# Kernel tuning notes

Measured on AMD Instinct MI355X. Metric: run time of the kernel, lower is better.

The kernel has to match this reference:

```python
import jax, jax.numpy as jnp
import numpy as np

B, S, D = 4, 2048, 2048
NQ, NKV = 16, 4
HD = D // NQ          # head_size = 128
GROUP = NQ // NKV     # 4


def _rope_table(seq_len, head_size, theta=10000.0):
    # [seq, head_size/2, 2] = (cos, sin), matching torch polar freqs_cis
    inv = 1.0 / (theta ** (np.arange(0, head_size, 2, dtype=np.float32) / head_size))
    ang = np.arange(seq_len, dtype=np.float32)[:, None] * inv[None, :]
    return jnp.asarray(np.stack([np.cos(ang), np.sin(ang)], axis=-1))


def setup_inputs() -> dict:
    key = jax.random.key(0)
    ks = jax.random.split(key, 6)
    sd = 0.02
    return {
        "x": jax.random.normal(ks[0], (B, S, D), jnp.float32),
        "freq_cis": _rope_table(S, HD),
        "Wq": jax.random.normal(ks[1], (D, NQ * HD), jnp.float32) * sd,
        "bq": jnp.zeros((NQ * HD,), jnp.float32),
        "Wk": jax.random.normal(ks[2], (D, NKV * HD), jnp.float32) * sd,
        "bk": jnp.zeros((NKV * HD,), jnp.float32),
        "Wv": jax.random.normal(ks[3], (D, NKV * HD), jnp.float32) * sd,
        "bv": jnp.zeros((NKV * HD,), jnp.float32),
        "Wo": jax.random.normal(ks[4], (NQ * HD, D), jnp.float32) * sd,
        "start_pos": 0,
    }


def _apply_rope(x, fc):
    # x: [b, s, h, d]; fc: [s, d/2, 2] -> complex multiply on (even, odd) pairs
    xr = x.reshape(*x.shape[:-1], -1, 2)
    cos = fc[None, :, None, :, 0]
    sin = fc[None, :, None, :, 1]
    x0, x1 = xr[..., 0], xr[..., 1]
    out = jnp.stack([x0 * cos - x1 * sin, x0 * sin + x1 * cos], axis=-1)
    return out.reshape(x.shape)


def reference(x, freq_cis, Wq, bq, Wk, bk, Wv, bv, Wo, start_pos):
    b, s, _ = x.shape
    q = (x @ Wq + bq).reshape(b, s, NQ, HD)
    k = (x @ Wk + bk).reshape(b, s, NKV, HD)
    v = (x @ Wv + bv).reshape(b, s, NKV, HD)

    fc = freq_cis[start_pos:start_pos + s]
    q = _apply_rope(q, fc)
    k = _apply_rope(k, fc)

    # [b, nkv, group, s, d] query view; k/v stay [b, nkv, s, d] (GQA broadcast)
    q = q.transpose(0, 2, 1, 3).reshape(b, NKV, GROUP, s, HD)
    k = k.transpose(0, 2, 1, 3)
    v = v.transpose(0, 2, 1, 3)

    scale = 1.0 / jnp.sqrt(jnp.asarray(HD, x.dtype))
    scores = jnp.einsum("bhgqd,bhkd->bhgqk", q, k) * scale
    causal = jnp.tril(jnp.ones((s, s), bool))
    scores = jnp.where(causal[None, None, None], scores, jnp.asarray(-jnp.inf, scores.dtype))
    probs = jax.nn.softmax(scores, axis=-1)
    o = jnp.einsum("bhgqk,bhkd->bhgqd", probs, v)

    o = o.reshape(b, NQ, s, HD).transpose(0, 2, 1, 3).reshape(b, s, NQ * HD)
    return o @ Wo
```

## Files before the change

### kernel.cpp

```cpp
#include <hip/hip_runtime.h>
#include <stdint.h>

typedef __attribute__((ext_vector_type(8))) short bf16x8;
typedef __attribute__((ext_vector_type(4))) float f32x4;
typedef __attribute__((ext_vector_type(16))) float f32x16;

#define S_LEN 2048
#define D_MODEL 2048
#define NQH 16
#define NKVH 4
#define HDIM 128
#define BATCH 4

__device__ __forceinline__ float bf2f(unsigned short s) {
  union { unsigned u; float f; } v; v.u = ((unsigned)s) << 16; return v.f;
}
__device__ __forceinline__ unsigned short f2bf(float f) {
  union { float f; unsigned u; } v; v.f = f;
  unsigned r = v.u + 0x7FFFu + ((v.u >> 16) & 1u);
  return (unsigned short)(r >> 16);
}
__device__ __forceinline__ f32x4 fzero() {
  f32x4 v; v[0]=0.f; v[1]=0.f; v[2]=0.f; v[3]=0.f; return v;
}
__device__ __forceinline__ void async16(const void* g, void* l) {
  __builtin_amdgcn_global_load_lds(
      (const __attribute__((address_space(1))) unsigned int*)g,
      (__attribute__((address_space(3))) unsigned int*)l, 16, 0, 0);
}
__device__ __forceinline__ unsigned cvtpk(float lo, float hi) {
  unsigned r;
  asm("v_cvt_pk_bf16_f32 %0, %1, %2" : "=v"(r) : "v"(lo), "v"(hi));
  return r;
}

__global__ void k_convert_x(const float* __restrict__ x, unsigned short* __restrict__ xb, int n4) {
  int stride = gridDim.x * blockDim.x;
  for (int i = blockIdx.x * blockDim.x + threadIdx.x; i < n4; i += stride) {
    float4 v = ((const float4*)x)[i];
    ushort4 o;
    o.x = f2bf(v.x); o.y = f2bf(v.y); o.z = f2bf(v.z); o.w = f2bf(v.w);
    ((ushort4*)xb)[i] = o;
  }
}

__global__ void k_transpose_all(const float* __restrict__ Wq, const float* __restrict__ Wk,
                                const float* __restrict__ Wv, const float* __restrict__ Wo,
                                unsigned short* __restrict__ Wt, unsigned short* __restrict__ Wot) {
  __shared__ float tile[32][33];
  int bid = blockIdx.x;
  const float* W; unsigned short* D; int N, nx;
  if (bid < 4096)      { W = Wq; D = Wt;                          N = 2048; nx = 64; }
  else if (bid < 5120) { W = Wk; D = Wt + (size_t)2048 * 2048;    N = 512;  nx = 16; bid -= 4096; }
  else if (bid < 6144) { W = Wv; D = Wt + (size_t)2560 * 2048;    N = 512;  nx = 16; bid -= 5120; }
  else                 { W = Wo; D = Wot;                         N = 2048; nx = 64; bid -= 6144; }
  int tx = threadIdx.x & 31, ty = threadIdx.x >> 5;
  int n0 = (bid % nx) * 32, k0 = (bid / nx) * 32;
  #pragma unroll
  for (int i = 0; i < 4; ++i)
    tile[ty + i*8][tx] = W[(size_t)(k0 + ty + i*8) * N + n0 + tx];
  __syncthreads();
  #pragma unroll
  for (int i = 0; i < 4; ++i)
    D[(size_t)(n0 + ty + i*8) * 2048 + k0 + tx] = f2bf(tile[tx][ty + i*8]);
}

__global__ void k_rope2(unsigned short* __restrict__ Qb, unsigned short* __restrict__ Kb,
                        const float* __restrict__ fc, const int* __restrict__ start_pos,
                        int nq, int ntot) {
  int sp = start_pos[0];
  int stride = gridDim.x * blockDim.x;
  for (int i = blockIdx.x * blockDim.x + threadIdx.x; i < ntot; i += stride) {
    unsigned* T = (i < nq) ? (unsigned*)Qb : (unsigned*)Kb;
    int idx = (i < nq) ? i : i - nq;
    int d2 = idx & 63;
    int s = (idx >> 6) & (S_LEN - 1);
    unsigned v = T[idx];
    float x0 = bf2f((unsigned short)(v & 0xFFFFu));
    float x1 = bf2f((unsigned short)(v >> 16));
    float c  = fc[((size_t)(sp + s) * 64 + d2) * 2];
    float sn = fc[((size_t)(sp + s) * 64 + d2) * 2 + 1];
    float y0 = x0 * c - x1 * sn;
    float y1 = x0 * sn + x1 * c;
    T[idx] = (unsigned)f2bf(y0) | ((unsigned)f2bf(y1) << 16);
  }
}

#define BARRIER() __builtin_amdgcn_s_barrier()
#define LGKM0()  do { asm volatile("s_waitcnt lgkmcnt(0)" ::: "memory"); \
                      __builtin_amdgcn_sched_barrier(0); } while (0)
#define VMCNT6() asm volatile("s_waitcnt vmcnt(6)" ::: "memory")
#define VMCNT4() asm volatile("s_waitcnt vmcnt(4)" ::: "memory")
#define VMCNT0() asm volatile("s_waitcnt vmcnt(0)" ::: "memory")

__device__ __forceinline__ bf16x8 ldsrd(const unsigned short* L, int row, int kk, int g) {
  int Xs = (kk * 64 + g * 16) ^ ((row & 7) << 4);
  return *(const bf16x8*)&L[row * 64 + (Xs >> 1)];
}
__device__ __forceinline__ void stage8(const unsigned short* __restrict__ G, int gbase,
                                       int k0, unsigned short* lds, int rowbase, int lane) {
  int row = rowbase + (lane >> 3);
  int col8 = (lane & 7) ^ ((lane >> 3) & 7);
  async16(G + (size_t)(gbase + row) * 2048 + k0 + col8 * 8, lds + rowbase * 64 + lane * 8);
}

__global__ __launch_bounds__(512, 2) void k_gemm_qkv(
    const unsigned short* __restrict__ A, const unsigned short* __restrict__ Bt,
    const float* __restrict__ bq, const float* __restrict__ bk, const float* __restrict__ bv,
    unsigned short* __restrict__ Qo, unsigned short* __restrict__ Ko, unsigned short* __restrict__ Vto)
{
  __shared__ __align__(16) unsigned short Ab[3][256 * 64];
  __shared__ __align__(16) unsigned short Bb[3][128 * 64];
  const int NT = 32, NXT = 24;
  const int tid = threadIdx.x, lane = tid & 63, w = tid >> 6;
  const int lr = lane & 15, g = lane >> 4;
  const int wm = w >> 1, wn = w & 1;

  int nwg = NXT * 32;
  int cpx = nwg >> 3;
  int bid = blockIdx.x;
  int swz = (bid & 7) * cpx + (bid >> 3);
  const int by = swz / NXT, bx = swz % NXT;
  const int mbase = by * 256, nbase = bx * 128;

  #define ST_A(tt) { unsigned short* L = Ab[(tt) % 3]; int k0 = (tt) * 64; \
    _Pragma("unroll") for (int it = 0; it < 4; ++it) { int c = tid + it * 512; \
      int row = c >> 3, col8 = (c & 7) ^ (row & 7); \
      async16(A + (size_t)(mbase + row) * 2048 + k0 + col8 * 8, L + c * 8); } }
  #define ST_B(tt) { unsigned short* L = Bb[(tt) % 3]; int k0 = (tt) * 64; \
    _Pragma("unroll") for (int it = 0; it < 2; ++it) { int c = tid + it * 512; \
      int row = c >> 3, col8 = (c & 7) ^ (row & 7); \
      async16(Bt + (size_t)(nbase + row) * 2048 + k0 + col8 * 8, L + c * 8); } }

  f32x4 acc[4][4];
  #pragma unroll
  for (int m = 0; m < 4; ++m)
    #pragma unroll
    for (int n = 0; n < 4; ++n) acc[m][n] = fzero();

  ST_A(0); ST_B(0); ST_A(1); ST_B(1);
  VMCNT6();
  BARRIER();

  for (int t = 0; t < NT; ++t) {
    const unsigned short* Al = Ab[t % 3];
    const unsigned short* Bl = Bb[t % 3];
    bf16x8 a[2][4], b[2][2];

    #pragma unroll
    for (int kk = 0; kk < 2; ++kk) {
      #pragma unroll
      for (int m = 0; m < 4; ++m) a[kk][m] = ldsrd(Al, wm * 64 + m * 16 + lr, kk, g);
      #pragma unroll
      for (int n = 0; n < 2; ++n) b[kk][n] = ldsrd(Bl, wn * 64 + n * 16 + lr, kk, g);
    }
    if (t + 2 < NT) ST_A(t + 2);
    BARRIER(); LGKM0();
    __builtin_amdgcn_s_setprio(1);
    #pragma unroll
    for (int kk = 0; kk < 2; ++kk)
      #pragma unroll
      for (int m = 0; m < 4; ++m)
        #pragma unroll
        for (int n = 0; n < 2; ++n)
          acc[m][n] = __builtin_amdgcn_mfma_f32_16x16x32_bf16(a[kk][m], b[kk][n], acc[m][n], 0, 0, 0);
    __builtin_amdgcn_s_setprio(0);
    BARRIER();

    #pragma unroll
    for (int kk = 0; kk < 2; ++kk)
      #pragma unroll
      for (int n = 0; n < 2; ++n) b[kk][n] = ldsrd(Bl, wn * 64 + (2 + n) * 16 + lr, kk, g);
    if (t + 2 < NT) { ST_B(t + 2); VMCNT6(); } else { VMCNT0(); }
    BARRIER(); LGKM0();
    __builtin_amdgcn_s_setprio(1);
    #pragma unroll
    for (int kk = 0; kk < 2; ++kk)
      #pragma unroll
      for (int m = 0; m < 4; ++m)
        #pragma unroll
        for (int n = 0; n < 2; ++n)
          acc[m][2 + n] = __builtin_amdgcn_mfma_f32_16x16x32_bf16(a[kk][m], b[kk][n], acc[m][2 + n], 0, 0, 0);
    __builtin_amdgcn_s_setprio(0);
    BARRIER();
  }

  const float SCL2E = 0.08838834764831845f * 1.4426950408889634f;
  #pragma unroll
  for (int n = 0; n < 4; ++n) {
    const int ng = nbase + wn * 64 + n * 16 + lr;
    const int seg = (ng < 2048) ? 0 : (ng < 2560 ? 1 : 2);
    const int nn = ng - (seg == 0 ? 0 : (seg == 1 ? 2048 : 2560));
    const int hh = nn >> 7, dd = nn & 127;
    const float bias = (seg == 0 ? bq[nn] : (seg == 1 ? bk[nn] : bv[nn]));
    #pragma unroll
    for (int m = 0; m < 4; ++m)
      #pragma unroll
      for (int i = 0; i < 4; ++i) {
        int mg = mbase + wm * 64 + m * 16 + g * 4 + i;
        int bb = mg >> 11, s = mg & 2047;
        float val = acc[m][n][i] + bias;
        if (seg == 0) {
          val *= SCL2E;
          Qo[((size_t)(bb * NQH + hh) * S_LEN + s) * HDIM + dd] = f2bf(val);
        } else if (seg == 1) {
          Ko[((size_t)(bb * NKVH + hh) * S_LEN + s) * HDIM + dd] = f2bf(val);
        } else {
          Vto[((size_t)(bb * NKVH + hh) * HDIM + dd) * S_LEN + s] = f2bf(val);
        }
      }
  }
  #undef ST_A
  #undef ST_B
}

__global__ __launch_bounds__(512, 2) void k_gemm_out256(
    const unsigned short* __restrict__ A, const unsigned short* __restrict__ Bt,
    float* __restrict__ Cf)
{
  __shared__ __align__(16) unsigned short Abuf[2][256 * 64];
  __shared__ __align__(16) unsigned short Bbuf[2][256 * 64];
  const int NT = 32, NXT = 8;
  const int tid = threadIdx.x, lane = tid & 63, w = tid >> 6;
  const int lr = lane & 15, g = lane >> 4;
  const int wm = w >> 2, wn = w & 3;

  int nwg = NXT * 32;
  int cpx = nwg >> 3;
  int bid = blockIdx.x;
  int swz = (bid & 7) * cpx + (bid >> 3);
  const int by = swz / NXT, bx = swz % NXT;
  const int mbase = by * 256, nbase = bx * 256;

  #define ST_AQ02(tt) if ((tt) < NT) { unsigned short* L = Abuf[(tt) & 1]; int k0 = (tt) * 64; \
    _Pragma("unroll") for (int it = 0; it < 2; ++it) { int sub = it * 8 + w; \
      stage8(A, mbase, k0, L, (sub >> 3) * 128 + (sub & 7) * 8, lane); } }
  #define ST_AQ13(tt) if ((tt) < NT) { unsigned short* L = Abuf[(tt) & 1]; int k0 = (tt) * 64; \
    _Pragma("unroll") for (int it = 0; it < 2; ++it) { int sub = it * 8 + w; \
      stage8(A, mbase, k0, L, 64 + (sub >> 3) * 128 + (sub & 7) * 8, lane); } }
  #define ST_BS0(tt) if ((tt) < NT) { unsigned short* L = Bbuf[(tt) & 1]; int k0 = (tt) * 64; \
    _Pragma("unroll") for (int it = 0; it < 2; ++it) { int sub = it * 8 + w; \
      stage8(Bt, nbase, k0, L, (sub >> 2) * 64 + (sub & 3) * 8, lane); } }
  #define ST_BS1(tt) if ((tt) < NT) { unsigned short* L = Bbuf[(tt) & 1]; int k0 = (tt) * 64; \
    _Pragma("unroll") for (int it = 0; it < 2; ++it) { int sub = it * 8 + w; \
      stage8(Bt, nbase, k0, L, 32 + (sub >> 2) * 64 + (sub & 3) * 8, lane); } }

  f32x4 acc[8][4];
  #pragma unroll
  for (int m = 0; m < 8; ++m)
    #pragma unroll
    for (int n = 0; n < 4; ++n) acc[m][n] = fzero();

  ST_AQ02(0); ST_AQ13(0); ST_BS0(0); ST_BS1(0);
  ST_AQ02(1); ST_BS1(1);
  VMCNT4();
  BARRIER();

  bf16x8 a[2][4], b[2][2];

  for (int t = 0; t < NT; ++t) {
    const unsigned short* Al = Abuf[t & 1];
    const unsigned short* Bl = Bbuf[t & 1];

    #pragma unroll
    for (int kk = 0; kk < 2; ++kk) {
      #pragma unroll
      for (int m = 0; m < 4; ++m) a[kk][m] = ldsrd(Al, wm * 128 + m * 16 + lr, kk, g);
      #pragma unroll
      for (int n = 0; n < 2; ++n) b[kk][n] = ldsrd(Bl, wn * 64 + n * 16 + lr, kk, g);
    }
    ST_AQ13(t + 1);
    BARRIER(); LGKM0();
    __builtin_amdgcn_s_setprio(1);
    #pragma unroll
    for (int kk = 0; kk < 2; ++kk)
      #pragma unroll
      for (int m = 0; m < 4; ++m)
        #pragma unroll
        for (int n = 0; n < 2; ++n)
          acc[m][n] = __builtin_amdgcn_mfma_f32_16x16x32_bf16(a[kk][m], b[kk][n], acc[m][n], 0, 0, 0);
    __builtin_amdgcn_s_setprio(0);
    BARRIER();

    #pragma unroll
    for (int kk = 0; kk < 2; ++kk)
      #pragma unroll
      for (int n = 0; n < 2; ++n) b[kk][n] = ldsrd(Bl, wn * 64 + (2 + n) * 16 + lr, kk, g);
    ST_BS0(t + 1);
    BARRIER(); LGKM0();
    __builtin_amdgcn_s_setprio(1);
    #pragma unroll
    for (int kk = 0; kk < 2; ++kk)
      #pragma unroll
      for (int m = 0; m < 4; ++m)
        #pragma unroll
        for (int n = 0; n < 2; ++n)
          acc[m][2 + n] = __builtin_amdgcn_mfma_f32_16x16x32_bf16(a[kk][m], b[kk][n], acc[m][2 + n], 0, 0, 0);
    __builtin_amdgcn_s_setprio(0);
    BARRIER();

    #pragma unroll
    for (int kk = 0; kk < 2; ++kk)
      #pragma unroll
      for (int m = 0; m < 4; ++m) a[kk][m] = ldsrd(Al, wm * 128 + 64 + m * 16 + lr, kk, g);
    ST_AQ02(t + 2);
    BARRIER(); LGKM0();
    __builtin_amdgcn_s_setprio(1);
    #pragma unroll
    for (int kk = 0; kk < 2; ++kk)
      #pragma unroll
      for (int m = 0; m < 4; ++m)
        #pragma unroll
        for (int n = 0; n < 2; ++n)
          acc[4 + m][2 + n] = __builtin_amdgcn_mfma_f32_16x16x32_bf16(a[kk][m], b[kk][n], acc[4 + m][2 + n], 0, 0, 0);
    __builtin_amdgcn_s_setprio(0);
    BARRIER();

    #pragma unroll
    for (int kk = 0; kk < 2; ++kk)
      #pragma unroll
      for (int n = 0; n < 2; ++n) b[kk][n] = ldsrd(Bl, wn * 64 + n * 16 + lr, kk, g);
    ST_BS1(t + 2);
    VMCNT4();
    BARRIER(); LGKM0();
    __builtin_amdgcn_s_setprio(1);
    #pragma unroll
    for (int kk = 0; kk < 2; ++kk)
      #pragma unroll
      for (int m = 0; m < 4; ++m)
        #pragma unroll
        for (int n = 0; n < 2; ++n)
          acc[4 + m][n] = __builtin_amdgcn_mfma_f32_16x16x32_bf16(a[kk][m], b[kk][n], acc[4 + m][n], 0, 0, 0);
    __builtin_amdgcn_s_setprio(0);
    BARRIER();
  }

  #pragma unroll
  for (int m = 0; m < 8; ++m)
    #pragma unroll
    for (int n = 0; n < 4; ++n)
      #pragma unroll
      for (int i = 0; i < 4; ++i) {
        int mg = mbase + wm * 128 + m * 16 + g * 4 + i;
        int ng = nbase + wn * 64 + n * 16 + lr;
        Cf[(size_t)mg * 2048 + ng] = acc[m][n][i];
      }
  #undef ST_AQ02
  #undef ST_AQ13
  #undef ST_BS0
  #undef ST_BS1
}

__global__ __launch_bounds__(512, 2) void k_flash2(
    const unsigned short* __restrict__ Q, const unsigned short* __restrict__ K,
    const unsigned short* __restrict__ Vt, unsigned short* __restrict__ O)
{
  __shared__ __align__(16) unsigned short SH[49152];

  const int tid = threadIdx.x;
  const int lane = tid & 63;
  const int w = tid >> 6;
  const int ql = lane & 31;
  const int hi = lane >> 5;

  const int bh = blockIdx.x >> 2;
  const int tp = blockIdx.x & 3;
  const int b = bh >> 4, h = bh & 15;
  const int kh = h >> 2;

  const unsigned short* Qbase = Q + (size_t)(b * NQH + h) * S_LEN * HDIM;
  const unsigned short* Kbase = K + (size_t)(b * NKVH + kh) * S_LEN * HDIM;
  const unsigned short* Vtb   = Vt + (size_t)(b * NKVH + kh) * HDIM * S_LEN;

  #define STAGEKV(jj) { unsigned short* Kd = SH + ((jj) % 3) * 16384; \
    unsigned short* Vd = Kd + 8192; \
    _Pragma("unroll") for (int it = 0; it < 2; ++it) { \
      int c = tid + it * 512; int row = c >> 4, col = c & 15; \
      int lcol = (col & 8) | ((col ^ (row & 7)) & 7); \
      async16(Kbase + (size_t)((jj) * 64 + row) * HDIM + lcol * 8, Kd + c * 8); } \
    _Pragma("unroll") for (int it = 0; it < 2; ++it) { \
      int c = tid + it * 512; int row = c >> 3, col = c & 7; \
      int lcol = col ^ (row & 7); \
      async16(Vtb + (size_t)row * S_LEN + (jj) * 64 + lcol * 8, Vd + c * 8); } }

  #pragma unroll 1
  for (int half = 0; half < 2; ++half) {
    const int t = half ? (7 - tp) : tp;
    const int nkv = 4 * t + 4;
    const int qg = t * 256 + w * 32 + ql;

    __syncthreads();

    bf16x8 qf[8];
    {
      const unsigned short* qp = Qbase + (size_t)qg * HDIM;
      #pragma unroll
      for (int dd = 0; dd < 8; ++dd)
        qf[dd] = *(const bf16x8*)(qp + dd * 16 + hi * 8);
    }

    float m_r = -1e30f, l_r = 0.f;
    f32x16 oA[4];
    #pragma unroll
    for (int db = 0; db < 4; ++db)
      #pragma unroll
      for (int r = 0; r < 16; ++r) oA[db][r] = 0.f;

    STAGEKV(0);
    STAGEKV(1);
    VMCNT4();
    BARRIER();

    for (int j = 0; j < nkv; ++j) {
      const unsigned short* Kl = SH + (j % 3) * 16384;
      const unsigned short* Vl = Kl + 8192;

      if (j + 2 < nkv) STAGEKV(j + 2);

      if (j * 64 <= t * 256 + w * 32 + 31) {
        f32x16 p0, p1;
        #pragma unroll
        for (int r = 0; r < 16; ++r) { p0[r] = 0.f; p1[r] = 0.f; }
        __builtin_amdgcn_s_setprio(1);
        #pragma unroll
        for (int dd = 0; dd < 8; ++dd) {
          const int off = (((dd * 32 + hi * 16) ^ ((ql & 7) << 4)) >> 1);
          bf16x8 a0 = *(const bf16x8*)&Kl[ql * 128 + off];
          bf16x8 a1 = *(const bf16x8*)&Kl[(32 + ql) * 128 + off];
          p0 = __builtin_amdgcn_mfma_f32_32x32x16_bf16(a0, qf[dd], p0, 0, 0, 0);
          p1 = __builtin_amdgcn_mfma_f32_32x32x16_bf16(a1, qf[dd], p1, 0, 0, 0);
        }
        __builtin_amdgcn_s_setprio(0);

        #pragma unroll
        for (int r = 0; r < 16; ++r) {
          const int kl = (r & 3) + 8 * (r >> 2);
          int kg = j * 64 + kl + 4 * hi;
          if (kg > qg) p0[r] = -1e30f;
          if (kg + 32 > qg) p1[r] = -1e30f;
        }

        float pm = -1e30f;
        #pragma unroll
        for (int r = 0; r < 16; ++r) pm = fmaxf(pm, fmaxf(p0[r], p1[r]));
        pm = fmaxf(pm, __shfl_xor(pm, 32));
        if (!__all(pm - m_r <= 8.0f)) {
          const float mn = fmaxf(m_r, pm);
          const float corr = exp2f(m_r - mn);
          m_r = mn;
          l_r *= corr;
          #pragma unroll
          for (int db = 0; db < 4; ++db)
            #pragma unroll
            for (int r = 0; r < 16; ++r) oA[db][r] *= corr;
        }
        float rs = 0.f;
        #pragma unroll
        for (int r = 0; r < 16; ++r) {
          p0[r] = exp2f(p0[r] - m_r);
          p1[r] = exp2f(p1[r] - m_r);
          rs += p0[r] + p1[r];
        }
        rs += __shfl_xor(rs, 32);
        l_r += rs;

        bf16x8 pb[4];
        {
          unsigned Wv[8], W2v[8];
          #pragma unroll
          for (int d = 0; d < 4; ++d) {
            Wv[d]      = cvtpk(p0[4*d],     p0[4*d + 1]);
            W2v[d]     = cvtpk(p0[4*d + 2], p0[4*d + 3]);
            Wv[4 + d]  = cvtpk(p1[4*d],     p1[4*d + 1]);
            W2v[4 + d] = cvtpk(p1[4*d + 2], p1[4*d + 3]);
          }
          #pragma unroll
          for (int kt = 0; kt < 2; ++kt) {
            #pragma unroll
            for (int s = 0; s < 2; ++s) {
              unsigned ownW   = hi ? Wv[kt*4 + 2*s + 1]  : Wv[kt*4 + 2*s];
              unsigned sendW  = hi ? Wv[kt*4 + 2*s]      : Wv[kt*4 + 2*s + 1];
              unsigned recvW  = (unsigned)__shfl_xor((int)sendW, 32);
              unsigned ownW2  = hi ? W2v[kt*4 + 2*s + 1] : W2v[kt*4 + 2*s];
              unsigned sendW2 = hi ? W2v[kt*4 + 2*s]     : W2v[kt*4 + 2*s + 1];
              unsigned recvW2 = (unsigned)__shfl_xor((int)sendW2, 32);
              union { unsigned u[4]; bf16x8 v; } pk;
              pk.u[0] = hi ? recvW  : ownW;
              pk.u[1] = hi ? recvW2 : ownW2;
              pk.u[2] = hi ? ownW   : recvW;
              pk.u[3] = hi ? ownW2  : recvW2;
              pb[kt*2 + s] = pk.v;
            }
          }
        }

        __builtin_amdgcn_s_setprio(1);
        #pragma unroll
        for (int ks = 0; ks < 4; ++ks) {
          #pragma unroll
          for (int db = 0; db < 4; ++db) {
            const int off = (((ks * 32 + hi * 16) ^ ((ql & 7) << 4)) >> 1);
            bf16x8 av = *(const bf16x8*)&Vl[(db * 32 + ql) * 64 + off];
            oA[db] = __builtin_amdgcn_mfma_f32_32x32x16_bf16(av, pb[ks], oA[db], 0, 0, 0);
          }
        }
        __builtin_amdgcn_s_setprio(0);
      }

      if (j + 2 < nkv) { VMCNT4(); }
      else if (j + 1 < nkv) { VMCNT0(); }
      BARRIER();
    }

    {
      const float invl = 1.f / l_r;
      const int qloc = w * 32 + ql;
      #pragma unroll
      for (int db = 0; db < 4; ++db)
        #pragma unroll
        for (int g4 = 0; g4 < 4; ++g4) {
          unsigned lo  = cvtpk(oA[db][g4*4 + 0] * invl, oA[db][g4*4 + 1] * invl);
          unsigned hi2 = cvtpk(oA[db][g4*4 + 2] * invl, oA[db][g4*4 + 3] * invl);
          int byteoff = qloc * 256 + ((db * 64 + g4 * 16 + hi * 8) ^ ((qloc & 7) << 4));
          *(uint2*)((char*)SH + byteoff) = make_uint2(lo, hi2);
        }
    }
    __syncthreads();
    {
      const int q2 = tid >> 1, hf = tid & 1;
      unsigned short* orow = O + ((size_t)(b * S_LEN + t * 256 + q2)) * D_MODEL + h * HDIM + hf * 64;
      #pragma unroll
      for (int u = 0; u < 8; ++u) {
        int byteoff = q2 * 256 + ((hf * 128 + u * 16) ^ ((q2 & 7) << 4));
        bf16x8 v = *(const bf16x8*)((const char*)SH + byteoff);
        *(bf16x8*)(orow + u * 8) = v;
      }
    }
  }
  #undef STAGEKV
}

extern "C" void kernel_launch(void* const* d_in, const int* in_sizes, int n_in,
                              void* d_out, int out_size, void* d_ws, size_t ws_size,
                              hipStream_t stream) {
  (void)in_sizes; (void)n_in; (void)out_size; (void)ws_size;
  const float* x  = (const float*)d_in[0];
  const float* fc = (const float*)d_in[1];
  const float* Wq = (const float*)d_in[2];
  const float* bq = (const float*)d_in[3];
  const float* Wk = (const float*)d_in[4];
  const float* bk = (const float*)d_in[5];
  const float* Wv = (const float*)d_in[6];
  const float* bv = (const float*)d_in[7];
  const float* Wo = (const float*)d_in[8];
  const int* start_pos = (const int*)d_in[9];
  float* out = (float*)d_out;

  unsigned short* ws = (unsigned short*)d_ws;
  size_t off = 0;
  unsigned short* xb  = ws + off; off += (size_t)8192 * 2048;
  unsigned short* Wt  = ws + off; off += (size_t)3072 * 2048;
  unsigned short* Wot = ws + off; off += (size_t)2048 * 2048;
  unsigned short* Qb  = ws + off; off += (size_t)BATCH * NQH  * S_LEN * HDIM;
  unsigned short* Kb  = ws + off; off += (size_t)BATCH * NKVH * S_LEN * HDIM;
  unsigned short* Vtb = ws + off; off += (size_t)BATCH * NKVH * S_LEN * HDIM;
  unsigned short* Ob  = ws + off; off += (size_t)8192 * 2048;

  k_convert_x<<<2048, 256, 0, stream>>>(x, xb, 8192 * 2048 / 4);
  k_transpose_all<<<10240, 256, 0, stream>>>(Wq, Wk, Wv, Wo, Wt, Wot);

  k_gemm_qkv<<<dim3(768), 512, 0, stream>>>(xb, Wt, bq, bk, bv, Qb, Kb, Vtb);

  k_rope2<<<2048, 256, 0, stream>>>(Qb, Kb, fc, start_pos,
                                    BATCH * NQH * S_LEN * 64,
                                    (BATCH * NQH + BATCH * NKVH) * S_LEN * 64);

  k_flash2<<<dim3(256), 512, 0, stream>>>(Qb, Kb, Vtb, Ob);

  k_gemm_out256<<<dim3(256), 512, 0, stream>>>(Ob, Wot, out);
}
```

Baseline: 373.6 us.

## Fuse Q RoPE into flash attention and shrink attention blocks to 128 queries

RoPE for Q now runs inside the flash kernel while Q fragments are loaded, so the separate pass no longer reads and writes Q through global memory. RoPE for K stays in a smaller standalone kernel. The flash kernel moves from 512 threads with 256-query tiles and triple-buffered KV to 256 threads with 128-query tiles, double buffering and a full barrier each iteration, and launches twice as many blocks. This trades Q global traffic and launch cost for a shallower prefetch pipeline, more barrier stalls, and extra RoPE arithmetic and fc loads in the attention kernel.

```diff
diff --git a/kernel.cpp b/kernel.cpp
--- a/kernel.cpp
+++ b/kernel.cpp
@@ -65,24 +65,21 @@
     D[(size_t)(n0 + ty + i*8) * 2048 + k0 + tx] = f2bf(tile[tx][ty + i*8]);
 }
 
-__global__ void k_rope2(unsigned short* __restrict__ Qb, unsigned short* __restrict__ Kb,
-                        const float* __restrict__ fc, const int* __restrict__ start_pos,
-                        int nq, int ntot) {
+__global__ void k_ropeK(unsigned short* __restrict__ Kb, const float* __restrict__ fc,
+                        const int* __restrict__ start_pos, int total) {
   int sp = start_pos[0];
   int stride = gridDim.x * blockDim.x;
-  for (int i = blockIdx.x * blockDim.x + threadIdx.x; i < ntot; i += stride) {
-    unsigned* T = (i < nq) ? (unsigned*)Qb : (unsigned*)Kb;
-    int idx = (i < nq) ? i : i - nq;
-    int d2 = idx & 63;
-    int s = (idx >> 6) & (S_LEN - 1);
-    unsigned v = T[idx];
+  for (int i = blockIdx.x * blockDim.x + threadIdx.x; i < total; i += stride) {
+    int d2 = i & 63;
+    int s = (i >> 6) & (S_LEN - 1);
+    unsigned v = ((unsigned*)Kb)[i];
     float x0 = bf2f((unsigned short)(v & 0xFFFFu));
     float x1 = bf2f((unsigned short)(v >> 16));
     float c  = fc[((size_t)(sp + s) * 64 + d2) * 2];
     float sn = fc[((size_t)(sp + s) * 64 + d2) * 2 + 1];
     float y0 = x0 * c - x1 * sn;
     float y1 = x0 * sn + x1 * c;
-    T[idx] = (unsigned)f2bf(y0) | ((unsigned)f2bf(y1) << 16);
+    ((unsigned*)Kb)[i] = (unsigned)f2bf(y0) | ((unsigned)f2bf(y1) << 16);
   }
 }
 
@@ -90,7 +87,6 @@
 #define LGKM0()  do { asm volatile("s_waitcnt lgkmcnt(0)" ::: "memory"); \
                       __builtin_amdgcn_sched_barrier(0); } while (0)
 #define VMCNT6() asm volatile("s_waitcnt vmcnt(6)" ::: "memory")
-#define VMCNT4() asm volatile("s_waitcnt vmcnt(4)" ::: "memory")
 #define VMCNT0() asm volatile("s_waitcnt vmcnt(0)" ::: "memory")
 
 __device__ __forceinline__ bf16x8 ldsrd(const unsigned short* L, int row, int kk, int g) {
@@ -253,7 +249,7 @@
 
   ST_AQ02(0); ST_AQ13(0); ST_BS0(0); ST_BS1(0);
   ST_AQ02(1); ST_BS1(1);
-  VMCNT4();
+  asm volatile("s_waitcnt vmcnt(4)" ::: "memory");
   BARRIER();
 
   bf16x8 a[2][4], b[2][2];
@@ -321,7 +317,7 @@
       #pragma unroll
       for (int n = 0; n < 2; ++n) b[kk][n] = ldsrd(Bl, wn * 64 + n * 16 + lr, kk, g);
     ST_BS1(t + 2);
-    VMCNT4();
+    asm volatile("s_waitcnt vmcnt(4)" ::: "memory");
     BARRIER(); LGKM0();
     __builtin_amdgcn_s_setprio(1);
     #pragma unroll
@@ -351,11 +347,12 @@
   #undef ST_BS1
 }
 
-__global__ __launch_bounds__(512, 2) void k_flash2(
+__global__ __launch_bounds__(256, 2) void k_flash2(
     const unsigned short* __restrict__ Q, const unsigned short* __restrict__ K,
-    const unsigned short* __restrict__ Vt, unsigned short* __restrict__ O)
+    const unsigned short* __restrict__ Vt, unsigned short* __restrict__ O,
+    const float* __restrict__ fc, const int* __restrict__ start_pos)
 {
-  __shared__ __align__(16) unsigned short SH[49152];
+  __shared__ __align__(16) unsigned short SH[32768];
 
   const int tid = threadIdx.x;
   const int lane = tid & 63;
@@ -363,40 +360,53 @@
   const int ql = lane & 31;
   const int hi = lane >> 5;
 
-  const int bh = blockIdx.x >> 2;
-  const int tp = blockIdx.x & 3;
+  const int bh = blockIdx.x >> 3;
+  const int tp = blockIdx.x & 7;
   const int b = bh >> 4, h = bh & 15;
   const int kh = h >> 2;
+  const int sp = start_pos[0];
 
   const unsigned short* Qbase = Q + (size_t)(b * NQH + h) * S_LEN * HDIM;
   const unsigned short* Kbase = K + (size_t)(b * NKVH + kh) * S_LEN * HDIM;
   const unsigned short* Vtb   = Vt + (size_t)(b * NKVH + kh) * HDIM * S_LEN;
 
-  #define STAGEKV(jj) { unsigned short* Kd = SH + ((jj) % 3) * 16384; \
+  #define STAGEKV(jj) { unsigned short* Kd = SH + ((jj) & 1) * 16384; \
     unsigned short* Vd = Kd + 8192; \
-    _Pragma("unroll") for (int it = 0; it < 2; ++it) { \
-      int c = tid + it * 512; int row = c >> 4, col = c & 15; \
+    _Pragma("unroll") for (int it = 0; it < 4; ++it) { \
+      int c = tid + it * 256; int row = c >> 4, col = c & 15; \
       int lcol = (col & 8) | ((col ^ (row & 7)) & 7); \
       async16(Kbase + (size_t)((jj) * 64 + row) * HDIM + lcol * 8, Kd + c * 8); } \
-    _Pragma("unroll") for (int it = 0; it < 2; ++it) { \
-      int c = tid + it * 512; int row = c >> 3, col = c & 7; \
+    _Pragma("unroll") for (int it = 0; it < 4; ++it) { \
+      int c = tid + it * 256; int row = c >> 3, col = c & 7; \
       int lcol = col ^ (row & 7); \
       async16(Vtb + (size_t)row * S_LEN + (jj) * 64 + lcol * 8, Vd + c * 8); } }
 
   #pragma unroll 1
   for (int half = 0; half < 2; ++half) {
-    const int t = half ? (7 - tp) : tp;
-    const int nkv = 4 * t + 4;
-    const int qg = t * 256 + w * 32 + ql;
+    const int t = half ? (15 - tp) : tp;
+    const int nkv = 2 * t + 2;
+    const int qg = t * 128 + w * 32 + ql;
 
     __syncthreads();
 
     bf16x8 qf[8];
     {
       const unsigned short* qp = Qbase + (size_t)qg * HDIM;
-      #pragma unroll
-      for (int dd = 0; dd < 8; ++dd)
-        qf[dd] = *(const bf16x8*)(qp + dd * 16 + hi * 8);
+      const float* fcrow = fc + (size_t)(sp + qg) * 128;
+      #pragma unroll
+      for (int dd = 0; dd < 8; ++dd) {
+        bf16x8 raw = *(const bf16x8*)(qp + dd * 16 + hi * 8);
+        int d2b = (dd * 16 + hi * 8) >> 1;
+        union { unsigned u[4]; bf16x8 v; } out;
+        #pragma unroll
+        for (int u2 = 0; u2 < 4; ++u2) {
+          float x0 = bf2f((unsigned short)raw[2 * u2]);
+          float x1 = bf2f((unsigned short)raw[2 * u2 + 1]);
+          float2 cs = *(const float2*)&fcrow[(d2b + u2) * 2];
+          out.u[u2] = cvtpk(x0 * cs.x - x1 * cs.y, x0 * cs.y + x1 * cs.x);
+        }
+        qf[dd] = out.v;
+      }
     }
 
     float m_r = -1e30f, l_r = 0.f;
@@ -407,17 +417,15 @@
       for (int r = 0; r < 16; ++r) oA[db][r] = 0.f;
 
     STAGEKV(0);
-    STAGEKV(1);
-    VMCNT4();
-    BARRIER();
+    __syncthreads();
 
     for (int j = 0; j < nkv; ++j) {
-      const unsigned short* Kl = SH + (j % 3) * 16384;
+      const unsigned short* Kl = SH + (j & 1) * 16384;
       const unsigned short* Vl = Kl + 8192;
 
-      if (j + 2 < nkv) STAGEKV(j + 2);
-
-      if (j * 64 <= t * 256 + w * 32 + 31) {
+      if (j + 1 < nkv) STAGEKV(j + 1);
+
+      if (j * 64 <= t * 128 + w * 32 + 31) {
         f32x16 p0, p1;
         #pragma unroll
         for (int r = 0; r < 16; ++r) { p0[r] = 0.f; p1[r] = 0.f; }
@@ -506,10 +514,7 @@
         }
         __builtin_amdgcn_s_setprio(0);
       }
-
-      if (j + 2 < nkv) { VMCNT4(); }
-      else if (j + 1 < nkv) { VMCNT0(); }
-      BARRIER();
+      __syncthreads();
     }
 
     {
@@ -528,7 +533,7 @@
     __syncthreads();
     {
       const int q2 = tid >> 1, hf = tid & 1;
-      unsigned short* orow = O + ((size_t)(b * S_LEN + t * 256 + q2)) * D_MODEL + h * HDIM + hf * 64;
+      unsigned short* orow = O + ((size_t)(b * S_LEN + t * 128 + q2)) * D_MODEL + h * HDIM + hf * 64;
       #pragma unroll
       for (int u = 0; u < 8; ++u) {
         int byteoff = q2 * 256 + ((hf * 128 + u * 16) ^ ((q2 & 7) << 4));
@@ -571,11 +576,9 @@
 
   k_gemm_qkv<<<dim3(768), 512, 0, stream>>>(xb, Wt, bq, bk, bv, Qb, Kb, Vtb);
 
-  k_rope2<<<2048, 256, 0, stream>>>(Qb, Kb, fc, start_pos,
-                                    BATCH * NQH * S_LEN * 64,
-                                    (BATCH * NQH + BATCH * NKVH) * S_LEN * 64);
-
-  k_flash2<<<dim3(256), 512, 0, stream>>>(Qb, Kb, Vtb, Ob);
+  k_ropeK<<<512, 256, 0, stream>>>(Kb, fc, start_pos, BATCH * NKVH * S_LEN * 64);
+
+  k_flash2<<<dim3(512), 256, 0, stream>>>(Qb, Kb, Vtb, Ob, fc, start_pos);
 
   k_gemm_out256<<<dim3(256), 512, 0, stream>>>(Ob, Wot, out);
 }
```

Result: no change. 370.6 us (-0.8%).
